# Optimization experiments

Measured on AMD Instinct MI355X. Metric: run time of the kernel, lower is better.

The kernel has to match this reference:

```python
import jax, jax.numpy as jnp
import numpy as np

N = 100000      # total nodes (100 graphs x 1000 nodes each)
G = 100         # graphs per batch
F_IN = 12       # node_features (temporal window)
F_OUT = 32      # DCRNN hidden size (hardcoded in module)
K = 5           # diffusion (Chebyshev) steps (hardcoded)
C = 4           # num_classes
E = 16 * N      # edges: ring (N) + random (15N)


def setup_inputs() -> dict:
    key = jax.random.key(0)
    ks = jax.random.split(key, 12)
    x = jax.random.normal(ks[0], (N, F_IN), dtype=jnp.float32)
    ring = jnp.arange(N, dtype=jnp.int32)
    src = jnp.concatenate([ring, jax.random.randint(ks[1], (15 * N,), 0, N, dtype=jnp.int32)])
    dst = jnp.concatenate([(ring + 1) % N, jax.random.randint(ks[2], (15 * N,), 0, N, dtype=jnp.int32)])
    edge_index = jnp.stack([src, dst])  # [2, E]
    edge_weight = jax.random.uniform(ks[3], (E,), dtype=jnp.float32, minval=0.1, maxval=1.0)
    batch = (jnp.arange(N, dtype=jnp.int32) * G) // N  # sorted graph ids, 1000 nodes per graph
    s = 0.1
    return dict(
        x=x, edge_index=edge_index, edge_weight=edge_weight, batch=batch,
        W_z=jax.random.normal(ks[4], (2, K, F_IN + F_OUT, F_OUT), jnp.float32) * s,
        b_z=jax.random.normal(ks[5], (F_OUT,), jnp.float32) * s,
        W_r=jax.random.normal(ks[6], (2, K, F_IN + F_OUT, F_OUT), jnp.float32) * s,
        b_r=jax.random.normal(ks[7], (F_OUT,), jnp.float32) * s,
        W_h=jax.random.normal(ks[8], (2, K, F_IN + F_OUT, F_OUT), jnp.float32) * s,
        b_h=jax.random.normal(ks[9], (F_OUT,), jnp.float32) * s,
        W_lin=jax.random.normal(ks[10], (F_OUT, C), jnp.float32) * s,
        b_lin=jax.random.normal(ks[11], (C,), jnp.float32) * s,
    )


def reference(x, edge_index, edge_weight, batch, W_z, b_z, W_r, b_r, W_h, b_h, W_lin, b_lin):
    row, col = edge_index[0], edge_index[1]
    # weighted in/out degrees (to_dense_adj sums duplicate edges, same as segment_sum)
    deg_out_inv = 1.0 / jax.ops.segment_sum(edge_weight, row, num_segments=N)
    deg_in_inv = 1.0 / jax.ops.segment_sum(edge_weight, col, num_segments=N)
    norm_out = deg_out_inv[row][:, None]  # per-edge 1/deg_out(src)
    norm_in = deg_in_inv[row][:, None]    # per-edge 1/deg_in(src), as in DConv

    def prop_fwd(h):  # out[dst] += h[src]/deg_out[src]
        return jax.ops.segment_sum(norm_out * h[row], col, num_segments=N)

    def prop_rev(h):  # reverse (transposed) diffusion: out[src] += h[dst]/deg_in[src]
        return jax.ops.segment_sum(norm_in * h[col], row, num_segments=N)

    def dconv(Xc, W, b):
        # Chebyshev diffusion conv, W: [2, K, F_in+F_out, F_out]
        H = Xc @ (W[0, 0] + W[1, 0])
        T1o, T1i = prop_fwd(Xc), prop_rev(Xc)
        H = H + T1o @ W[0, 1] + T1i @ W[1, 1]
        T0o = T0i = Xc
        for k in range(2, K):
            T2o = 2.0 * prop_fwd(T1o) - T0o
            T2i = 2.0 * prop_rev(T1i) - T0i
            H = H + T2o @ W[0, k] + T2i @ W[1, k]
            T0o, T1o = T1o, T2o
            T0i, T1i = T1i, T2i
        return H + b

    # GRU gating with zero-initialized hidden state (H=None in module)
    Hst = jnp.zeros((N, F_OUT), x.dtype)
    XH = jnp.concatenate([x, Hst], axis=1)
    Z = jax.nn.sigmoid(dconv(XH, W_z, b_z))
    R = jax.nn.sigmoid(dconv(XH, W_r, b_r))
    XRH = jnp.concatenate([x, R * Hst], axis=1)
    H_tilde = jnp.tanh(dconv(XRH, W_h, b_h))
    H = Z * Hst + (1.0 - Z) * H_tilde

    h = jax.nn.relu(H) @ W_lin + b_lin            # [N, C]
    sums = jax.ops.segment_sum(h, batch, num_segments=G)
    counts = jax.ops.segment_sum(jnp.ones((N,), h.dtype), batch, num_segments=G)
    return sums / counts[:, None]                 # global_mean_pool -> [G, C]
```

## Files before the change

### kernel.cpp

```cpp
#include <hip/hip_runtime.h>
#include <math.h>

#define NN    100000
#define GG    100
#define FIN   12
#define FOUT  32
#define KD    5
#define CC    4
#define EE    1600000
#define ROWS  108
#define NBF   782
#define NBINS 1564
#define NBC   1024
#define CHUNK 1563
#define NSEG  (NBINS * NBC)

__device__ __forceinline__ unsigned bfr(float f) {
    unsigned u = __float_as_uint(f);
    return (u + 0x7FFFu + ((u >> 16) & 1u)) >> 16;
}
__device__ __forceinline__ unsigned pack2(float a, float b) {
    return bfr(a) | (bfr(b) << 16);
}
#define BLO(u) __uint_as_float((u) << 16)
#define BHI(u) __uint_as_float((u) & 0xFFFF0000u)

__device__ __forceinline__ int chunk_of_block(int b) {
    return ((b & 7) << 7) | (b >> 3);
}


__global__ __launch_bounds__(256) void k_hist(const int* __restrict__ ei,
                                              int* __restrict__ hist_g) {
    __shared__ int hist[NBINS];
    for (int i = threadIdx.x; i < NBINS; i += 256) hist[i] = 0;
    __syncthreads();
    int chunk = chunk_of_block(blockIdx.x);
    int lo = chunk * CHUNK, hi = lo + CHUNK;
    if (hi > EE) hi = EE;
    for (int e = lo + threadIdx.x; e < hi; e += 256) {
        int s = ei[e], d = ei[EE + e];
        atomicAdd(&hist[d >> 7], 1);
        atomicAdd(&hist[NBF + (s >> 7)], 1);
    }
    __syncthreads();
    for (int i = threadIdx.x; i < NBINS; i += 256)
        hist_g[i * NBC + chunk] = hist[i];
}

__global__ __launch_bounds__(1024) void k_scan1(int* __restrict__ g,
                                                int* __restrict__ bsum) {
    __shared__ int sh[1024];
    int t = threadIdx.x;
    int i = blockIdx.x * 1024 + t;
    int v = g[i];
    sh[t] = v;
    __syncthreads();
    for (int d = 1; d < 1024; d <<= 1) {
        int x = sh[t];
        if (t >= d) x += sh[t - d];
        __syncthreads();
        sh[t] = x;
        __syncthreads();
    }
    g[i] = sh[t] - v;
    if (t == 1023) bsum[blockIdx.x] = sh[1023];
}

__global__ __launch_bounds__(1024) void k_scan2(int* __restrict__ bsum, int nb) {
    __shared__ int sh[1024];
    int t = threadIdx.x;
    int a = (2 * t     < nb) ? bsum[2 * t]     : 0;
    int b = (2 * t + 1 < nb) ? bsum[2 * t + 1] : 0;
    int s = a + b;
    sh[t] = s;
    __syncthreads();
    for (int d = 1; d < 1024; d <<= 1) {
        int x = sh[t];
        if (t >= d) x += sh[t - d];
        __syncthreads();
        sh[t] = x;
        __syncthreads();
    }
    int base = sh[t] - s;
    if (2 * t < nb)     bsum[2 * t] = base;
    if (2 * t + 1 < nb) bsum[2 * t + 1] = base + a;
}

__global__ __launch_bounds__(1024) void k_scan3(int* __restrict__ g,
                                                const int* __restrict__ bsum,
                                                int* __restrict__ off,
                                                int* __restrict__ off_node) {
    int i = blockIdx.x * 1024 + threadIdx.x;
    int v = g[i] + bsum[blockIdx.x];
    g[i] = v;
    if ((i & (NBC - 1)) == 0) off[i / NBC] = v;
    if (i == 0) { off[NBINS] = 2 * EE; off_node[2 * NN] = 2 * EE; }
}

__global__ __launch_bounds__(256) void k_place(const int* __restrict__ ei,
                                               const float* __restrict__ ew,
                                               const int* __restrict__ base_g,
                                               int2* __restrict__ recA) {
    __shared__ int cur[NBINS];
    int chunk = chunk_of_block(blockIdx.x);
    for (int i = threadIdx.x; i < NBINS; i += 256) cur[i] = base_g[i * NBC + chunk];
    __syncthreads();
    int lo = chunk * CHUNK, hi = lo + CHUNK;
    if (hi > EE) hi = EE;
    for (int e = lo + threadIdx.x; e < hi; e += 256) {
        int s = ei[e], d = ei[EE + e];
        float w = ew[e];
        int pf = atomicAdd(&cur[d >> 7], 1);
        recA[pf] = make_int2(s | ((d & 127) << 17), __float_as_int(w));
        int pr = atomicAdd(&cur[NBF + (s >> 7)], 1);
        recA[pr] = make_int2(d | ((s & 127) << 17), __float_as_int(w));
    }
}

__global__ __launch_bounds__(256) void k_subcsr(
        const int* __restrict__ off, const int2* __restrict__ recA,
        const float* __restrict__ x,
        int* __restrict__ off_node, int* __restrict__ rec2,
        float* __restrict__ dinv_in, float* __restrict__ dinv_out,
        uint2* __restrict__ gA) {
    __shared__ int   hist[128];
    __shared__ int   lofs[128];
    __shared__ int   cur[128];
    __shared__ float wsum[128];
    __shared__ float dl[128];
    int b = blockIdx.x;
    int t = threadIdx.x;
    if (t < 128) { hist[t] = 0; wsum[t] = 0.f; }
    __syncthreads();
    int e0 = off[b], e1 = off[b + 1];
    for (int e = e0 + t; e < e1; e += 256) {
        int2 r = recA[e];
        int loc = r.x >> 17;
        atomicAdd(&hist[loc], 1);
        atomicAdd(&wsum[loc], __int_as_float(r.y));
    }
    __syncthreads();
    if (t < 128) lofs[t] = hist[t];
    __syncthreads();
    for (int d = 1; d < 128; d <<= 1) {
        int v = 0;
        if (t < 128 && t >= d) v = lofs[t - d];
        __syncthreads();
        if (t < 128) lofs[t] += v;
        __syncthreads();
    }
    bool rev = b >= NBF;
    int base = (rev ? b - NBF : b) * 128;
    if (t < 128) {
        int ex = lofs[t] - hist[t];
        lofs[t] = ex;
        cur[t] = 0;
        int node = base + t;
        if (node < NN) {
            off_node[(rev ? NN : 0) + node] = e0 + ex;
            float inv = 1.f / wsum[t];
            dl[t] = inv;
            if (rev) dinv_out[node] = inv;
            else     dinv_in[node]  = inv;
        }
    }
    __syncthreads();
    for (int e = e0 + t; e < e1; e += 256) {
        int rx = recA[e].x;
        int loc = rx >> 17;
        int pos = e0 + lofs[loc] + atomicAdd(&cur[loc], 1);
        rec2[pos] = rx & 0x1FFFF;
    }
    if (rev) {
        __syncthreads();
        for (int i = t; i < 128 * 3; i += 256) {
            int loc = i / 3, cc = i - loc * 3;
            int node = base + loc;
            if (node < NN) {
                float4 v = *(const float4*)(x + (size_t)node * FIN + cc * 4);
                float sc = dl[loc];
                gA[(size_t)node * 3 + cc] =
                    make_uint2(pack2(v.x * sc, v.y * sc), pack2(v.z * sc, v.w * sc));
            }
        }
    }
}


__global__ void k_misc(const float* __restrict__ Wz_in, const float* __restrict__ Wh_in,
                       float* __restrict__ Wz, float* __restrict__ Wh,
                       const float* __restrict__ b_lin, float* __restrict__ out,
                       const float* __restrict__ x, uint2* __restrict__ xb) {
    int t = blockIdx.x * 256 + threadIdx.x;
    if (t < 2 * ROWS * FOUT) {
        int sel = t / (ROWS * FOUT);
        int rem = t - sel * ROWS * FOUT;
        int r = rem / FOUT;
        int f = rem - r * FOUT;
        int b = r / 12;
        int i = r - b * 12;
        const float* Ws = sel ? Wh_in : Wz_in;
        float v;
        if (b == 0)
            v = Ws[(0 * KD + 0) * 44 * 32 + i * 32 + f] + Ws[(1 * KD + 0) * 44 * 32 + i * 32 + f];
        else if (b <= 4)
            v = Ws[(0 * KD + b) * 44 * 32 + i * 32 + f];
        else
            v = Ws[(1 * KD + (b - 4)) * 44 * 32 + i * 32 + f];
        (sel ? Wh : Wz)[r * FOUT + f] = v;
    }
    int u = t - 2 * ROWS * FOUT;
    if (u >= 0 && u < GG * CC) out[u] = b_lin[u & 3];
    if (t < 3 * NN) {
        int n = t / 3, c = t - n * 3;
        float4 v = *(const float4*)(x + (size_t)n * FIN + c * 4);
        xb[(size_t)n * 3 + c] = make_uint2(pack2(v.x, v.y), pack2(v.z, v.w));
    }
}

#define LREC 2048
__global__ __launch_bounds__(256) void k_gather(
        const int* __restrict__ off_node, const int* __restrict__ rec2,
        const uint2* __restrict__ gIn, const uint2* __restrict__ hIn,
        const uint2* __restrict__ prevF, const uint2* __restrict__ prevR,
        const float* __restrict__ dinv_in, const float* __restrict__ dinv_out,
        uint2* __restrict__ outF, uint2* __restrict__ outR,
        uint2* __restrict__ gOut, float c) {
    __shared__ int lrec[LREC];
    int xcd = blockIdx.x & 7;
    int grp = blockIdx.x >> 3;
    bool rev = xcd >= 4;
    int dbase = rev ? NN : 0;
    int ub = (grp * 4 + (xcd & 3)) * 256;
    int lin = ub + threadIdx.x;

    int u1 = ub + 255; if (u1 > 3 * NN - 1) u1 = 3 * NN - 1;
    int node0 = ub / 3, node1 = u1 / 3;
    int w0 = off_node[dbase + node0];
    int w1 = off_node[dbase + node1 + 1];
    int wn = w1 - w0;
    bool useLds = (wn <= LREC);
    if (useLds) {
        for (int i = threadIdx.x; i < wn; i += 256) lrec[i] = rec2[w0 + i];
    }
    __syncthreads();

    if (lin < 3 * NN) {
        int node = lin / 3;
        int ch = lin - node * 3;
        int i0 = dbase + node;
        int e0 = off_node[i0], e1 = off_node[i0 + 1];
        const uint2* in = rev ? hIn : gIn;

        float ax = 0.f, ay = 0.f, az = 0.f, aw = 0.f;
        float bx = 0.f, by = 0.f, bz = 0.f, bw = 0.f;
        if (useLds) {
            int a0 = e0 - w0, a1 = e1 - w0;
            int e = a0;
            for (; e + 7 < a1; e += 8) {
                int n0 = lrec[e],     n1 = lrec[e + 1], n2 = lrec[e + 2], n3 = lrec[e + 3];
                int n4 = lrec[e + 4], n5 = lrec[e + 5], n6 = lrec[e + 6], n7 = lrec[e + 7];
                uint2 v0 = in[(size_t)n0 * 3 + ch];
                uint2 v1 = in[(size_t)n1 * 3 + ch];
                uint2 v2 = in[(size_t)n2 * 3 + ch];
                uint2 v3 = in[(size_t)n3 * 3 + ch];
                uint2 v4 = in[(size_t)n4 * 3 + ch];
                uint2 v5 = in[(size_t)n5 * 3 + ch];
                uint2 v6 = in[(size_t)n6 * 3 + ch];
                uint2 v7 = in[(size_t)n7 * 3 + ch];
                ax += BLO(v0.x); ay += BHI(v0.x); az += BLO(v0.y); aw += BHI(v0.y);
                bx += BLO(v1.x); by += BHI(v1.x); bz += BLO(v1.y); bw += BHI(v1.y);
                ax += BLO(v2.x); ay += BHI(v2.x); az += BLO(v2.y); aw += BHI(v2.y);
                bx += BLO(v3.x); by += BHI(v3.x); bz += BLO(v3.y); bw += BHI(v3.y);
                ax += BLO(v4.x); ay += BHI(v4.x); az += BLO(v4.y); aw += BHI(v4.y);
                bx += BLO(v5.x); by += BHI(v5.x); bz += BLO(v5.y); bw += BHI(v5.y);
                ax += BLO(v6.x); ay += BHI(v6.x); az += BLO(v6.y); aw += BHI(v6.y);
                bx += BLO(v7.x); by += BHI(v7.x); bz += BLO(v7.y); bw += BHI(v7.y);
            }
            for (; e < a1; ++e) {
                int n0 = lrec[e];
                uint2 v0 = in[(size_t)n0 * 3 + ch];
                ax += BLO(v0.x); ay += BHI(v0.x); az += BLO(v0.y); aw += BHI(v0.y);
            }
        } else {
            for (int e = e0; e < e1; ++e) {
                int n0 = rec2[e];
                uint2 v0 = in[(size_t)n0 * 3 + ch];
                ax += BLO(v0.x); ay += BHI(v0.x); az += BLO(v0.y); aw += BHI(v0.y);
            }
        }
        ax += bx; ay += by; az += bz; aw += bw;

        float sc = rev ? c * dinv_in[node] : c;
        ax *= sc; ay *= sc; az *= sc; aw *= sc;

        size_t o = (size_t)node * 3 + ch;
        if (prevF) {
            uint2 p = (rev ? prevR : prevF)[o];
            ax -= BLO(p.x); ay -= BHI(p.x); az -= BLO(p.y); aw -= BHI(p.y);
        }
        (rev ? outR : outF)[o] = make_uint2(pack2(ax, ay), pack2(az, aw));
        if (!rev && gOut) {
            float g = dinv_out[node];
            gOut[o] = make_uint2(pack2(g * ax, g * ay), pack2(g * az, g * aw));
        }
    }
}


__global__ __launch_bounds__(256) void k_fused(
        const float* __restrict__ x, const uint2* __restrict__ TS2,
        const float* __restrict__ Wz, const float* __restrict__ Wh,
        const float* __restrict__ bz, const float* __restrict__ bh,
        const float* __restrict__ Wlin, float* __restrict__ out) {
    __shared__ float rows[128][13];
    __shared__ float red[256 * CC];
    int g = blockIdx.x >> 3;
    int seg = blockIdx.x & 7;
    int base = g * 1000 + seg * 125;
    int tid = threadIdx.x;
    int lane = tid & 63;
    int wave = tid >> 6;
    int f0 = __builtin_amdgcn_readfirstlane(wave * 8);

    float az0[8], ah0[8], az1[8], ah1[8];
#pragma unroll
    for (int fi = 0; fi < 8; ++fi) {
        float vz = bz[f0 + fi], vh = bh[f0 + fi];
        az0[fi] = vz; ah0[fi] = vh; az1[fi] = vz; ah1[fi] = vh;
    }
    bool act1 = (lane + 64) < 125;

    for (int b = 0; b < 9; ++b) {
        __syncthreads();
        if (b == 0) {
            const float* src = x + (size_t)base * FIN;
            for (int q = tid; q < 375; q += 256) {
                float4 v = *(const float4*)(src + q * 4);
                int e = q * 4;
                int n0 = e / 12,       i0 = e - n0 * 12;       rows[n0][i0] = v.x;
                int n1 = (e + 1) / 12, i1 = (e + 1) - n1 * 12; rows[n1][i1] = v.y;
                int n2 = (e + 2) / 12, i2 = (e + 2) - n2 * 12; rows[n2][i2] = v.z;
                int n3 = (e + 3) / 12, i3 = (e + 3) - n3 * 12; rows[n3][i3] = v.w;
            }
        } else {
            const uint2* Tb = TS2 + (size_t)(b - 1) * NN * 3;
            for (int q = tid; q < 375; q += 256) {
                int n = q / 3, cc = q - n * 3;
                uint2 v = Tb[(size_t)(base + n) * 3 + cc];
                rows[n][cc * 4 + 0] = BLO(v.x);
                rows[n][cc * 4 + 1] = BHI(v.x);
                rows[n][cc * 4 + 2] = BLO(v.y);
                rows[n][cc * 4 + 3] = BHI(v.y);
            }
        }
        __syncthreads();
        const float* wzr = Wz + b * 12 * FOUT + f0;
        const float* whr = Wh + b * 12 * FOUT + f0;
#pragma unroll
        for (int i = 0; i < FIN; ++i) {
            float v0 = rows[lane][i];
            float v1 = rows[lane + 64][i];
#pragma unroll
            for (int fi = 0; fi < 8; ++fi) {
                float wz = wzr[i * FOUT + fi];
                float wh = whr[i * FOUT + fi];
                az0[fi] = fmaf(v0, wz, az0[fi]);
                az1[fi] = fmaf(v1, wz, az1[fi]);
                ah0[fi] = fmaf(v0, wh, ah0[fi]);
                ah1[fi] = fmaf(v1, wh, ah1[fi]);
            }
        }
    }

    float o[CC] = {0.f, 0.f, 0.f, 0.f};
#pragma unroll
    for (int fi = 0; fi < 8; ++fi) {
        float z = 1.f / (1.f + __expf(-az0[fi]));
        float e2 = __expf(2.f * ah0[fi]);
        float th = 1.f - 2.f / (e2 + 1.f);
        float hv = fmaxf((1.f - z) * th, 0.f);
#pragma unroll
        for (int c = 0; c < CC; ++c) o[c] = fmaf(hv, Wlin[(f0 + fi) * 4 + c], o[c]);
    }
    if (act1) {
#pragma unroll
        for (int fi = 0; fi < 8; ++fi) {
            float z = 1.f / (1.f + __expf(-az1[fi]));
            float e2 = __expf(2.f * ah1[fi]);
            float th = 1.f - 2.f / (e2 + 1.f);
            float hv = fmaxf((1.f - z) * th, 0.f);
#pragma unroll
            for (int c = 0; c < CC; ++c) o[c] = fmaf(hv, Wlin[(f0 + fi) * 4 + c], o[c]);
        }
    }

#pragma unroll
    for (int c = 0; c < CC; ++c) red[tid * CC + c] = o[c];
    __syncthreads();
    for (int st = 128; st > 0; st >>= 1) {
        if (tid < st) {
#pragma unroll
            for (int c = 0; c < CC; ++c) red[tid * CC + c] += red[(tid + st) * CC + c];
        }
        __syncthreads();
    }
    if (tid == 0) {
#pragma unroll
        for (int c = 0; c < CC; ++c) atomicAdd(out + g * CC + c, red[c] * 0.001f);
    }
}


extern "C" void kernel_launch(void* const* d_in, const int* in_sizes, int n_in,
                              void* d_out, int out_size, void* d_ws, size_t ws_size,
                              hipStream_t stream) {
    const float* x     = (const float*)d_in[0];
    const int*   ei    = (const int*)d_in[1];
    const float* ew    = (const float*)d_in[2];
    const float* W_z   = (const float*)d_in[4];
    const float* b_z   = (const float*)d_in[5];
    const float* W_h   = (const float*)d_in[8];
    const float* b_h   = (const float*)d_in[9];
    const float* W_lin = (const float*)d_in[10];
    const float* b_lin = (const float*)d_in[11];
    float* out = (float*)d_out;

    int*   rec2     = (int*)d_ws;
    unsigned* TSb   = (unsigned*)(rec2 + 2 * (size_t)EE);
    int2*  recA     = (int2*)TSb;
    int*   hist_g   = rec2;
    int*   bsumS    = rec2 + NSEG;
    unsigned* gAu   = TSb + (size_t)8 * NN * 6 + 1600000;
    unsigned* gBu   = gAu + (size_t)NN * 6;
    unsigned* xbu   = gBu + (size_t)NN * 6;
    float* dinv_in  = (float*)(xbu + (size_t)NN * 6);
    float* dinv_out = dinv_in + NN;
    float* Wz       = dinv_out + NN;
    float* Wh       = Wz + ROWS * FOUT;
    int*   off      = (int*)(Wh + ROWS * FOUT);
    int*   off_node = off + NBINS + 1;

    uint2* TS2 = (uint2*)TSb;
    uint2* T1o = TS2 + (size_t)0 * NN * 3;
    uint2* T2o = TS2 + (size_t)1 * NN * 3;
    uint2* T3o = TS2 + (size_t)2 * NN * 3;
    uint2* T4o = TS2 + (size_t)3 * NN * 3;
    uint2* T1i = TS2 + (size_t)4 * NN * 3;
    uint2* T2i = TS2 + (size_t)5 * NN * 3;
    uint2* T3i = TS2 + (size_t)6 * NN * 3;
    uint2* T4i = TS2 + (size_t)7 * NN * 3;
    uint2* gA = (uint2*)gAu;
    uint2* gB = (uint2*)gBu;
    uint2* xb = (uint2*)xbu;

    dim3 B(256);
    int nbG = 2344;
    int nbScan = NSEG / 1024;
    int nbMisc = (3 * NN + 255) / 256;

    k_hist<<<NBC, B, 0, stream>>>(ei, hist_g);
    k_scan1<<<nbScan, 1024, 0, stream>>>(hist_g, bsumS);
    k_scan2<<<1, 1024, 0, stream>>>(bsumS, nbScan);
    k_scan3<<<nbScan, 1024, 0, stream>>>(hist_g, bsumS, off, off_node);
    k_place<<<NBC, B, 0, stream>>>(ei, ew, hist_g, recA);
    k_subcsr<<<NBINS, B, 0, stream>>>(off, recA, x, off_node, rec2, dinv_in, dinv_out, gA);

    k_misc<<<nbMisc, B, 0, stream>>>(W_z, W_h, Wz, Wh, b_lin, out, x, xb);

    k_gather<<<nbG, B, 0, stream>>>(off_node, rec2, gA, xb,  nullptr, nullptr, dinv_in, dinv_out, T1o, T1i, gB, 1.f);
    k_gather<<<nbG, B, 0, stream>>>(off_node, rec2, gB, T1i, xb,      xb,      dinv_in, dinv_out, T2o, T2i, gA, 2.f);
    k_gather<<<nbG, B, 0, stream>>>(off_node, rec2, gA, T2i, T1o,     T1i,     dinv_in, dinv_out, T3o, T3i, gB, 2.f);
    k_gather<<<nbG, B, 0, stream>>>(off_node, rec2, gB, T3i, T2o,     T2i,     dinv_in, dinv_out, T4o, T4i, nullptr, 2.f);

    k_fused<<<8 * GG, B, 0, stream>>>(x, TS2, Wz, Wh, b_z, b_h, W_lin, out);
}
```

Measured before the change: 310.5 us.

## Partition edge-placement histogram by XCD so scatter writes stay XCD-local

Reorders the global histogram layout so it is indexed by (xcd, bin, seq) instead of (bin, chunk). Each XCD's blocks then write recA into their own contiguous runs per bin, which is meant to cut cross-XCD cache-line sharing during the atomic-placement scatter. To keep the per-bin record groups usable, two small kernels are added to compute per-bin totals and offsets. k_subcsr now walks eight runs per bin instead of one contiguous range. This costs two extra launches and more fragmented reads in k_subcsr.

After: 316.9 us. 1.02x slower.

```diff
diff --git a/kernel.cpp b/kernel.cpp
--- a/kernel.cpp
+++ b/kernel.cpp
@@ -25,17 +25,14 @@
 #define BLO(u) __uint_as_float((u) << 16)
 #define BHI(u) __uint_as_float((u) & 0xFFFF0000u)
 
-__device__ __forceinline__ int chunk_of_block(int b) {
-    return ((b & 7) << 7) | (b >> 3);
-}
-
 
 __global__ __launch_bounds__(256) void k_hist(const int* __restrict__ ei,
                                               int* __restrict__ hist_g) {
     __shared__ int hist[NBINS];
     for (int i = threadIdx.x; i < NBINS; i += 256) hist[i] = 0;
     __syncthreads();
-    int chunk = chunk_of_block(blockIdx.x);
+    int xcd = blockIdx.x & 7, seq = blockIdx.x >> 3;
+    int chunk = (xcd << 7) | seq;
     int lo = chunk * CHUNK, hi = lo + CHUNK;
     if (hi > EE) hi = EE;
     for (int e = lo + threadIdx.x; e < hi; e += 256) {
@@ -45,7 +42,7 @@
     }
     __syncthreads();
     for (int i = threadIdx.x; i < NBINS; i += 256)
-        hist_g[i * NBC + chunk] = hist[i];
+        hist_g[(xcd * NBINS + i) * 128 + seq] = hist[i];
 }
 
 __global__ __launch_bounds__(1024) void k_scan1(int* __restrict__ g,
@@ -88,23 +85,61 @@
 }
 
 __global__ __launch_bounds__(1024) void k_scan3(int* __restrict__ g,
-                                                const int* __restrict__ bsum,
-                                                int* __restrict__ off,
-                                                int* __restrict__ off_node) {
+                                                const int* __restrict__ bsum) {
     int i = blockIdx.x * 1024 + threadIdx.x;
-    int v = g[i] + bsum[blockIdx.x];
-    g[i] = v;
-    if ((i & (NBC - 1)) == 0) off[i / NBC] = v;
-    if (i == 0) { off[NBINS] = 2 * EE; off_node[2 * NN] = 2 * EE; }
+    g[i] += bsum[blockIdx.x];
+}
+
+__global__ void k_binsum(const int* __restrict__ S, int* __restrict__ runsS,
+                         int* __restrict__ cnt) {
+    int b = blockIdx.x * 256 + threadIdx.x;
+    if (b >= NBINS) return;
+    int c = 0;
+#pragma unroll
+    for (int x = 0; x < 8; ++x) {
+        int st = S[(x * NBINS + b) * 128];
+        runsS[x * NBINS + b] = st;
+        int en;
+        if (b + 1 < NBINS)      en = S[(x * NBINS + b + 1) * 128];
+        else if (x < 7)         en = S[((x + 1) * NBINS) * 128];
+        else                    en = 2 * EE;
+        c += en - st;
+    }
+    cnt[b] = c;
+}
+
+__global__ __launch_bounds__(1024) void k_scanoff(const int* __restrict__ cnt,
+                                                  int* __restrict__ off,
+                                                  int* __restrict__ off_node) {
+    __shared__ int sh[1024];
+    int t = threadIdx.x;
+    int a = (2 * t     < NBINS) ? cnt[2 * t]     : 0;
+    int b = (2 * t + 1 < NBINS) ? cnt[2 * t + 1] : 0;
+    int s = a + b;
+    sh[t] = s;
+    __syncthreads();
+    for (int d = 1; d < 1024; d <<= 1) {
+        int x = sh[t];
+        if (t >= d) x += sh[t - d];
+        __syncthreads();
+        sh[t] = x;
+        __syncthreads();
+    }
+    int base = sh[t] - s;
+    if (2 * t < NBINS)     off[2 * t] = base;
+    if (2 * t + 1 < NBINS) off[2 * t + 1] = base + a;
+    if (t == 1023) { off[NBINS] = 2 * EE; off_node[2 * NN] = 2 * EE; }
 }
 
 __global__ __launch_bounds__(256) void k_place(const int* __restrict__ ei,
                                                const float* __restrict__ ew,
-                                               const int* __restrict__ base_g,
+                                               const int* __restrict__ S,
                                                int2* __restrict__ recA) {
     __shared__ int cur[NBINS];
-    int chunk = chunk_of_block(blockIdx.x);
-    for (int i = threadIdx.x; i < NBINS; i += 256) cur[i] = base_g[i * NBC + chunk];
+    int xcd = blockIdx.x & 7, seq = blockIdx.x >> 3;
+    int chunk = (xcd << 7) | seq;
+    for (int i = threadIdx.x; i < NBINS; i += 256)
+        cur[i] = S[(xcd * NBINS + i) * 128 + seq];
     __syncthreads();
     int lo = chunk * CHUNK, hi = lo + CHUNK;
     if (hi > EE) hi = EE;
@@ -119,11 +154,12 @@
 }
 
 __global__ __launch_bounds__(256) void k_subcsr(
-        const int* __restrict__ off, const int2* __restrict__ recA,
-        const float* __restrict__ x,
+        const int* __restrict__ off, const int* __restrict__ runsS,
+        const int2* __restrict__ recA, const float* __restrict__ x,
         int* __restrict__ off_node, int* __restrict__ rec2,
         float* __restrict__ dinv_in, float* __restrict__ dinv_out,
         uint2* __restrict__ gA) {
+    __shared__ int   rs[8], re[8];
     __shared__ int   hist[128];
     __shared__ int   lofs[128];
     __shared__ int   cur[128];
@@ -132,13 +168,21 @@
     int b = blockIdx.x;
     int t = threadIdx.x;
     if (t < 128) { hist[t] = 0; wsum[t] = 0.f; }
-    __syncthreads();
-    int e0 = off[b], e1 = off[b + 1];
-    for (int e = e0 + t; e < e1; e += 256) {
-        int2 r = recA[e];
-        int loc = r.x >> 17;
-        atomicAdd(&hist[loc], 1);
-        atomicAdd(&wsum[loc], __int_as_float(r.y));
+    if (t < 8) {
+        int x8 = t;
+        rs[t] = runsS[x8 * NBINS + b];
+        if (b + 1 < NBINS)  re[t] = runsS[x8 * NBINS + b + 1];
+        else if (x8 < 7)    re[t] = runsS[(x8 + 1) * NBINS];
+        else                re[t] = 2 * EE;
+    }
+    __syncthreads();
+    for (int r = 0; r < 8; ++r) {
+        for (int e = rs[r] + t; e < re[r]; e += 256) {
+            int2 rr = recA[e];
+            int loc = rr.x >> 17;
+            atomicAdd(&hist[loc], 1);
+            atomicAdd(&wsum[loc], __int_as_float(rr.y));
+        }
     }
     __syncthreads();
     if (t < 128) lofs[t] = hist[t];
@@ -152,6 +196,7 @@
     }
     bool rev = b >= NBF;
     int base = (rev ? b - NBF : b) * 128;
+    int e0 = off[b];
     if (t < 128) {
         int ex = lofs[t] - hist[t];
         lofs[t] = ex;
@@ -166,11 +211,13 @@
         }
     }
     __syncthreads();
-    for (int e = e0 + t; e < e1; e += 256) {
-        int rx = recA[e].x;
-        int loc = rx >> 17;
-        int pos = e0 + lofs[loc] + atomicAdd(&cur[loc], 1);
-        rec2[pos] = rx & 0x1FFFF;
+    for (int r = 0; r < 8; ++r) {
+        for (int e = rs[r] + t; e < re[r]; e += 256) {
+            int rx = recA[e].x;
+            int loc = rx >> 17;
+            int pos = e0 + lofs[loc] + atomicAdd(&cur[loc], 1);
+            rec2[pos] = rx & 0x1FFFF;
+        }
     }
     if (rev) {
         __syncthreads();
@@ -432,6 +479,7 @@
     int2*  recA     = (int2*)TSb;
     int*   hist_g   = rec2;
     int*   bsumS    = rec2 + NSEG;
+    int*   cnt      = bsumS + 2048;
     unsigned* gAu   = TSb + (size_t)8 * NN * 6 + 1600000;
     unsigned* gBu   = gAu + (size_t)NN * 6;
     unsigned* xbu   = gBu + (size_t)NN * 6;
@@ -441,6 +489,7 @@
     float* Wh       = Wz + ROWS * FOUT;
     int*   off      = (int*)(Wh + ROWS * FOUT);
     int*   off_node = off + NBINS + 1;
+    int*   runsS    = off_node + 2 * NN + 1;
 
     uint2* TS2 = (uint2*)TSb;
     uint2* T1o = TS2 + (size_t)0 * NN * 3;
@@ -463,9 +512,12 @@
     k_hist<<<NBC, B, 0, stream>>>(ei, hist_g);
     k_scan1<<<nbScan, 1024, 0, stream>>>(hist_g, bsumS);
     k_scan2<<<1, 1024, 0, stream>>>(bsumS, nbScan);
-    k_scan3<<<nbScan, 1024, 0, stream>>>(hist_g, bsumS, off, off_node);
+    k_scan3<<<nbScan, 1024, 0, stream>>>(hist_g, bsumS);
+    k_binsum<<<(NBINS + 255) / 256, B, 0, stream>>>(hist_g, runsS, cnt);
+    k_scanoff<<<1, 1024, 0, stream>>>(cnt, off, off_node);
     k_place<<<NBC, B, 0, stream>>>(ei, ew, hist_g, recA);
-    k_subcsr<<<NBINS, B, 0, stream>>>(off, recA, x, off_node, rec2, dinv_in, dinv_out, gA);
+    k_subcsr<<<NBINS, B, 0, stream>>>(off, runsS, recA, x, off_node, rec2,
+                                      dinv_in, dinv_out, gA);
 
     k_misc<<<nbMisc, B, 0, stream>>>(W_z, W_h, Wz, Wh, b_lin, out, x, xb);
 
```
